# Kernel tuning notes

Measured on AMD Instinct MI355X. Metric: run time of the kernel, lower is better.

## Reference

```python
import jax, jax.numpy as jnp
import numpy as np

N = 500_000    # total nodes across batched ligands
E = 2_000_000  # directed edges (avg degree 4)
G = 16_384     # number of graphs
ND, ED, H, EMB = 44, 12, 64, 128


def setup_inputs() -> dict:
    key = jax.random.key(0)
    ks = jax.random.split(key, 16)

    def w(k, shape, fan_in):
        return jax.random.normal(k, shape, jnp.float32) * (1.0 / np.sqrt(fan_in))

    return {
        "x": jax.random.normal(ks[0], (N, ND), jnp.float32),
        "edge_attr": jax.random.normal(ks[1], (E, ED), jnp.float32),
        "edge_index": jax.random.randint(ks[2], (2, E), 0, N, jnp.int32),
        "batch": jnp.sort(jax.random.randint(ks[3], (N,), 0, G, jnp.int32)),
        # GINEConv 1: edge lin (ED->ND), nn1: ND->64->64
        "el1_w": w(ks[4], (ED, ND), ED), "el1_b": jnp.zeros((ND,), jnp.float32),
        "w1a": w(ks[5], (ND, H), ND),   "b1a": jnp.zeros((H,), jnp.float32),
        "w1b": w(ks[6], (H, H), H),     "b1b": jnp.zeros((H,), jnp.float32),
        # GINEConv 2: edge lin (ED->64), nn2: 64->128->128
        "el2_w": w(ks[7], (ED, H), ED), "el2_b": jnp.zeros((H,), jnp.float32),
        "w2a": w(ks[8], (H, EMB), H),   "b2a": jnp.zeros((EMB,), jnp.float32),
        "w2b": w(ks[9], (EMB, EMB), EMB), "b2b": jnp.zeros((EMB,), jnp.float32),
    }


def _mlp(h, Wa, ba, Wb, bb):
    return jax.nn.relu(h @ Wa + ba) @ Wb + bb


def _gine(x, edge_attr, src, dst, ew, eb, Wa, ba, Wb, bb):
    # message = ReLU(x_j + Linear(edge_attr)); aggregate = scatter-add at target i
    msg = jax.nn.relu(x[src] + edge_attr @ ew + eb)          # [E, d]
    agg = jax.ops.segment_sum(msg, dst, num_segments=x.shape[0])
    # eps = 0 (default, train_eps=False): (1+eps)*x + agg == x + agg
    return _mlp(x + agg, Wa, ba, Wb, bb)


def reference(x, edge_attr, edge_index, batch,
              el1_w, el1_b, w1a, b1a, w1b, b1b,
              el2_w, el2_b, w2a, b2a, w2b, b2b):
    src, dst = edge_index[0], edge_index[1]
    h = jax.nn.relu(_gine(x, edge_attr, src, dst, el1_w, el1_b, w1a, b1a, w1b, b1b))
    h = _gine(h, edge_attr, src, dst, el2_w, el2_b, w2a, b2a, w2b, b2b)
    # global mean pool over graphs
    sums = jax.ops.segment_sum(h, batch, num_segments=G)                 # [G, EMB]
    cnt = jax.ops.segment_sum(jnp.ones((h.shape[0], 1), h.dtype), batch, num_segments=G)
    return sums / jnp.maximum(cnt, 1.0)
```

## Files before the change

### kernel.cpp

```cpp
#include <hip/hip_runtime.h>
#include <hip/hip_bf16.h>

#define NN 500000
#define EE 2000000
#define GG 16384
#define ND 44
#define ED 12
#define HH 64
#define EMB 128
#define NBLK 123
#define NTILE (NN / 16)

typedef __attribute__((ext_vector_type(8))) short bf16x8;
typedef __attribute__((ext_vector_type(4))) float f32x4;
typedef __attribute__((ext_vector_type(2))) _Float16 h2v;

__device__ inline short f2bf(float v) {
    unsigned int x = __builtin_bit_cast(unsigned int, v);
    x += 0x7FFFu + ((x >> 16) & 1u);
    return (short)(x >> 16);
}
__device__ inline unsigned short f2h(float v) {
    return __builtin_bit_cast(unsigned short, (_Float16)v);
}
__device__ inline float h2f(unsigned short s) {
    return (float)__builtin_bit_cast(_Float16, s);
}
__device__ inline unsigned pkh(float a, float b) {
    return (unsigned)f2h(a) | ((unsigned)f2h(b) << 16);
}
__device__ inline float2 upk(unsigned u) {
    return make_float2((float)__builtin_bit_cast(_Float16, (unsigned short)(u & 0xffffu)),
                       (float)__builtin_bit_cast(_Float16, (unsigned short)(u >> 16)));
}
__device__ inline float hdot2(unsigned a, unsigned b, float c) {
#if __has_builtin(__builtin_amdgcn_fdot2)
    return __builtin_amdgcn_fdot2(__builtin_bit_cast(h2v, a),
                                  __builtin_bit_cast(h2v, b), c, false);
#else
    float2 av = upk(a), bv = upk(b);
    return fmaf(av.y, bv.y, fmaf(av.x, bv.x, c));
#endif
}

__device__ inline void wave_lds_fence() {
    asm volatile("s_waitcnt lgkmcnt(0)" ::: "memory");
    __builtin_amdgcn_sched_barrier(0);
}

__global__ __launch_bounds__(256) void prep_weights(
    const float* __restrict__ w1a, const float* __restrict__ w1b,
    const float* __restrict__ w2a, const float* __restrict__ w2b,
    short* __restrict__ o) {
    int t = blockIdx.x * 256 + threadIdx.x;
    if (t < 4096) {
        int n = t >> 6, k = t & 63;
        o[t] = f2bf(k < ND ? w1a[k * HH + n] : 0.f);
    } else if (t < 8192) {
        int u = t - 4096; int n = u >> 6, k = u & 63;
        o[t] = f2bf(w1b[k * HH + n]);
    } else if (t < 16384) {
        int u = t - 8192; int n = u >> 6, k = u & 63;
        o[t] = f2bf(w2a[k * EMB + n]);
    } else if (t < 32768) {
        int u = t - 16384; int n = u >> 7, k = u & 127;
        o[t] = f2bf(w2b[k * EMB + n]);
    }
}

__global__ __launch_bounds__(256) void x_to_h(const float* __restrict__ x,
                                             unsigned short* __restrict__ xh) {
    for (long long t = (long long)(blockIdx.x) * 256 + threadIdx.x;
         t < (long long)NN * 64; t += (long long)gridDim.x * 256) {
        int i = (int)(t >> 6), c = (int)(t & 63);
        xh[t] = (c < ND) ? f2h(x[(size_t)i * ND + c]) : (unsigned short)0;
    }
}

__global__ __launch_bounds__(256) void hist_kernel(const int* __restrict__ ei,
                                                   int* __restrict__ deg) {
    int e = blockIdx.x * 256 + threadIdx.x;
    if (e < EE) atomicAdd(&deg[ei[EE + e]], 1);
}

__global__ __launch_bounds__(256) void scan_reduce(const int* __restrict__ deg,
                                                   int* __restrict__ bsum) {
    int b = blockIdx.x, t = threadIdx.x;
    int base = b * 4096;
    int s = 0;
    for (int i = t; i < 4096; i += 256) {
        int g = base + i;
        if (g < NN) s += deg[g];
    }
#pragma unroll
    for (int off = 32; off; off >>= 1) s += __shfl_xor(s, off);
    __shared__ int ws[4];
    if ((t & 63) == 0) ws[t >> 6] = s;
    __syncthreads();
    if (t == 0) bsum[b] = ws[0] + ws[1] + ws[2] + ws[3];
}

__global__ __launch_bounds__(128) void scan_mid(const int* __restrict__ bsum,
                                                int* __restrict__ boff,
                                                int* __restrict__ rowptr) {
    int t = threadIdx.x;
    int v = (t < NBLK) ? bsum[t] : 0;
    int x = v;
#pragma unroll
    for (int off = 1; off < 64; off <<= 1) {
        int y = __shfl_up(x, off);
        if ((t & 63) >= off) x += y;
    }
    __shared__ int wt[2];
    if ((t & 63) == 63) wt[t >> 6] = x;
    __syncthreads();
    int xx = x + ((t >= 64) ? wt[0] : 0);
    if (t < NBLK) boff[t] = xx - v;
    if (t == 127) rowptr[NN] = xx;
}

__global__ __launch_bounds__(256) void scan_final(const int* __restrict__ deg,
                                                  const int* __restrict__ boff,
                                                  int* __restrict__ rowptr,
                                                  int* __restrict__ cursor) {
    int b = blockIdx.x, t = threadIdx.x;
    int base = b * 4096 + t * 16;
    int loc[16];
    int s = 0;
#pragma unroll
    for (int j = 0; j < 16; ++j) {
        int g = base + j;
        loc[j] = (g < NN) ? deg[g] : 0;
        s += loc[j];
    }
    int xinc = s;
#pragma unroll
    for (int off = 1; off < 64; off <<= 1) {
        int y = __shfl_up(xinc, off);
        if ((t & 63) >= off) xinc += y;
    }
    __shared__ int wt[4];
    if ((t & 63) == 63) wt[t >> 6] = xinc;
    __syncthreads();
    int wv = t >> 6, woff = 0;
#pragma unroll
    for (int k = 0; k < 4; ++k)
        if (k < wv) woff += wt[k];
    int run = boff[b] + woff + (xinc - s);
#pragma unroll
    for (int j = 0; j < 16; ++j) {
        int g = base + j;
        if (g < NN) { rowptr[g] = run; cursor[g] = run; }
        run += loc[j];
    }
}

__global__ __launch_bounds__(256) void scatter_kernel(const int* __restrict__ ei,
                                                      const float* __restrict__ ea,
                                                      int* __restrict__ cursor,
                                                      unsigned int* __restrict__ csr) {
    int e = blockIdx.x * 256 + threadIdx.x;
    if (e < EE) {
        int dst = ei[EE + e];
        const float4* s = (const float4*)(ea + (size_t)e * ED);
        float4 a0 = s[0], a1 = s[1], a2 = s[2];
        uint4 P0, P1;
        P0.x = pkh(a0.x, a0.y); P0.y = pkh(a0.z, a0.w);
        P0.z = pkh(a1.x, a1.y); P0.w = pkh(a1.z, a1.w);
        P1.x = pkh(a2.x, a2.y); P1.y = pkh(a2.z, a2.w);
        P1.z = (unsigned)ei[e];
        P1.w = 0u;
        int pos = atomicAdd(&cursor[dst], 1);
        uint4* d = (uint4*)(csr + (size_t)pos * 8);
        d[0] = P0; d[1] = P1;
    }
}

template <int D>
__global__ __launch_bounds__(256) void agg_gather(
    const unsigned short* __restrict__ xh,
    const unsigned int* __restrict__ cea,
    const float* __restrict__ ew, const float* __restrict__ eb,
    const int* __restrict__ rowptr,
    short* __restrict__ out) {
    int lane = threadIdx.x & 63;
    int wv = threadIdx.x >> 6;
    int i0 = (blockIdx.x * 4 + wv) * 8;
    if (i0 >= NN) return;
    unsigned wp0, wp1, wp2, wp3, wp4, wp5;
    float breg;
    if (D == 64 || lane < D) {
        wp0 = pkh(ew[0 * D + lane], ew[1 * D + lane]);
        wp1 = pkh(ew[2 * D + lane], ew[3 * D + lane]);
        wp2 = pkh(ew[4 * D + lane], ew[5 * D + lane]);
        wp3 = pkh(ew[6 * D + lane], ew[7 * D + lane]);
        wp4 = pkh(ew[8 * D + lane], ew[9 * D + lane]);
        wp5 = pkh(ew[10 * D + lane], ew[11 * D + lane]);
        breg = eb[lane];
    } else {
        wp0 = wp1 = wp2 = wp3 = wp4 = wp5 = 0u; breg = 0.f;
    }
    int rp = (lane <= 8) ? rowptr[i0 + lane] : 0;
    int beg = __builtin_amdgcn_readfirstlane(__builtin_amdgcn_readlane(rp, 0));
    int end = __builtin_amdgcn_readfirstlane(__builtin_amdgcn_readlane(rp, 8));
    int s0 = 0, s1 = 0;
    if (beg + lane < end) s0 = (int)cea[(size_t)(beg + lane) * 8 + 6];
    if (beg + 64 + lane < end) s1 = (int)cea[(size_t)(beg + 64 + lane) * 8 + 6];

    auto SKIPLD = [&](int j) -> float {
        return h2f(xh[(size_t)(i0 + j) * 64 + lane]);
    };

    float acc = 0.f;
    int np = 0;
    int nb = __builtin_amdgcn_readlane(rp, 1);
    float sk = SKIPLD(0);
    while (np < 8 && nb == beg) {
        out[(size_t)(i0 + np) * 64 + lane] = f2bf(sk);
        ++np;
        nb = (np < 8) ? __builtin_amdgcn_readlane(rp, np + 1) : 0x7fffffff;
        sk = (np < 8) ? SKIPLD(np) : 0.f;
    }

    auto LOADE = [&](int pos, uint4& P0, uint2& P1, unsigned short& XR) {
        int p = pos < end ? pos : end - 1;
        int off = p - beg;
        int src;
        if (off < 64)       src = __builtin_amdgcn_readlane(s0, off);
        else if (off < 128) src = __builtin_amdgcn_readlane(s1, off - 64);
        else                src = __builtin_amdgcn_readfirstlane((int)cea[(size_t)p * 8 + 6]);
        P0 = *(const uint4*)(cea + (size_t)p * 8);
        P1 = *(const uint2*)(cea + (size_t)p * 8 + 4);
        XR = xh[(size_t)src * 64 + lane];
    };
    auto CONSUME = [&](int pos, const uint4& P0, const uint2& P1, unsigned short XR) {
        if (pos < end) {
            float elin = breg;
            elin = hdot2(P0.x, wp0, elin);
            elin = hdot2(P0.y, wp1, elin);
            elin = hdot2(P0.z, wp2, elin);
            elin = hdot2(P0.w, wp3, elin);
            elin = hdot2(P1.x, wp4, elin);
            elin = hdot2(P1.y, wp5, elin);
            acc += fmaxf(h2f(XR) + elin, 0.f);
            int p1 = pos + 1;
            if (p1 == nb) {
                do {
                    out[(size_t)(i0 + np) * 64 + lane] = f2bf(acc + sk);
                    acc = 0.f; ++np;
                    nb = (np < 8) ? __builtin_amdgcn_readlane(rp, np + 1) : 0x7fffffff;
                    sk = (np < 8) ? SKIPLD(np) : 0.f;
                } while (p1 == nb);
            }
        }
    };

    if (beg >= end) return;

    uint4 A0, B0, C0, D0, E0, F0, G0, H0;
    uint2 A1, B1, C1, D1, E1, F1, G1, H1;
    unsigned short Ax, Bx, Cx, Dx, Ex, Fx, Gx, Hx;
    int base = beg;
    LOADE(base + 0, A0, A1, Ax);
    LOADE(base + 1, B0, B1, Bx);
    LOADE(base + 2, C0, C1, Cx);
    LOADE(base + 3, D0, D1, Dx);
    LOADE(base + 4, E0, E1, Ex);
    LOADE(base + 5, F0, F1, Fx);
    LOADE(base + 6, G0, G1, Gx);
    LOADE(base + 7, H0, H1, Hx);
    __builtin_amdgcn_sched_barrier(0);
    while (base < end) {
        CONSUME(base + 0, A0, A1, Ax);
        CONSUME(base + 1, B0, B1, Bx);
        LOADE(base + 8, A0, A1, Ax);
        LOADE(base + 9, B0, B1, Bx);
        __builtin_amdgcn_sched_barrier(0);
        if (base + 2 >= end) break;
        CONSUME(base + 2, C0, C1, Cx);
        CONSUME(base + 3, D0, D1, Dx);
        LOADE(base + 10, C0, C1, Cx);
        LOADE(base + 11, D0, D1, Dx);
        __builtin_amdgcn_sched_barrier(0);
        if (base + 4 >= end) break;
        CONSUME(base + 4, E0, E1, Ex);
        CONSUME(base + 5, F0, F1, Fx);
        LOADE(base + 12, E0, E1, Ex);
        LOADE(base + 13, F0, F1, Fx);
        __builtin_amdgcn_sched_barrier(0);
        if (base + 6 >= end) break;
        CONSUME(base + 6, G0, G1, Gx);
        CONSUME(base + 7, H0, H1, Hx);
        LOADE(base + 14, G0, G1, Gx);
        LOADE(base + 15, H0, H1, Hx);
        __builtin_amdgcn_sched_barrier(0);
        base += 8;
    }
}

#define HSTR1 68
__global__ __launch_bounds__(256, 3) void mlp1(
    const short* __restrict__ ain,
    const short* __restrict__ w1a_t, const float* __restrict__ b1a,
    const short* __restrict__ w1b_t, const float* __restrict__ b1b,
    unsigned short* __restrict__ h) {
    __shared__ float hid[4][16 * HSTR1];
    int lane = threadIdx.x & 63;
    int wv = threadIdx.x >> 6;
    int mrow = lane & 15, q = lane >> 4;
    float* hw = hid[wv];

    bf16x8 wa[4][2], wb[4][2];
    float ba[4], bb[4];
#pragma unroll
    for (int nt = 0; nt < 4; ++nt) {
        int n = nt * 16 + mrow;
        ba[nt] = b1a[n]; bb[nt] = b1b[n];
#pragma unroll
        for (int s = 0; s < 2; ++s) {
            wa[nt][s] = *(const bf16x8*)(w1a_t + n * 64 + s * 32 + q * 8);
            wb[nt][s] = *(const bf16x8*)(w1b_t + n * 64 + s * 32 + q * 8);
        }
    }

    int tile = blockIdx.x * 4 + wv;
    int stride = gridDim.x * 4;
    if (tile >= NTILE) return;
    bf16x8 a0 = *(const bf16x8*)(ain + (size_t)(tile * 16 + mrow) * 64 + q * 8);
    bf16x8 a1 = *(const bf16x8*)(ain + (size_t)(tile * 16 + mrow) * 64 + 32 + q * 8);
    while (true) {
        int nxt = tile + stride;
        bool more = nxt < NTILE;
        bf16x8 na0{}, na1{};
        if (more) {
            na0 = *(const bf16x8*)(ain + (size_t)(nxt * 16 + mrow) * 64 + q * 8);
            na1 = *(const bf16x8*)(ain + (size_t)(nxt * 16 + mrow) * 64 + 32 + q * 8);
        }
        int node0 = tile * 16;
#pragma unroll
        for (int nt = 0; nt < 4; ++nt) {
            f32x4 acc = {ba[nt], ba[nt], ba[nt], ba[nt]};
            acc = __builtin_amdgcn_mfma_f32_16x16x32_bf16(a0, wa[nt][0], acc, 0, 0, 0);
            acc = __builtin_amdgcn_mfma_f32_16x16x32_bf16(a1, wa[nt][1], acc, 0, 0, 0);
            int n = nt * 16 + mrow;
#pragma unroll
            for (int r = 0; r < 4; ++r)
                hw[(q * 4 + r) * HSTR1 + n] = fmaxf(acc[r], 0.f);
        }
        wave_lds_fence();
        bf16x8 af2[2];
#pragma unroll
        for (int s = 0; s < 2; ++s) {
            f32x4 v0 = *(const f32x4*)(hw + mrow * HSTR1 + s * 32 + q * 8);
            f32x4 v1 = *(const f32x4*)(hw + mrow * HSTR1 + s * 32 + q * 8 + 4);
#pragma unroll
            for (int j = 0; j < 4; ++j) { af2[s][j] = f2bf(v0[j]); af2[s][j + 4] = f2bf(v1[j]); }
        }
#pragma unroll
        for (int nt = 0; nt < 4; ++nt) {
            f32x4 acc = {bb[nt], bb[nt], bb[nt], bb[nt]};
            acc = __builtin_amdgcn_mfma_f32_16x16x32_bf16(af2[0], wb[nt][0], acc, 0, 0, 0);
            acc = __builtin_amdgcn_mfma_f32_16x16x32_bf16(af2[1], wb[nt][1], acc, 0, 0, 0);
            int n = nt * 16 + mrow;
#pragma unroll
            for (int r = 0; r < 4; ++r)
                h[(size_t)(node0 + q * 4 + r) * HH + n] = f2h(fmaxf(acc[r], 0.f));
        }
        if (!more) break;
        tile = nxt; a0 = na0; a1 = na1;
        wave_lds_fence();
    }
}

#define HSTR2 132
#define WLSTR 136
__global__ __launch_bounds__(256, 2) void mlp2(
    const short* __restrict__ ain,
    const short* __restrict__ w2a_t, const float* __restrict__ b2a,
    const short* __restrict__ w2b_t, const float* __restrict__ b2b,
    const int* __restrict__ batch, float* __restrict__ sums) {
    __shared__ float buf[4][16 * HSTR2];
    __shared__ short wlds[EMB * WLSTR];
    int lane = threadIdx.x & 63;
    int wv = threadIdx.x >> 6;
    int mrow = lane & 15, q = lane >> 4;
    float* bw = buf[wv];

    for (int idx = threadIdx.x * 8; idx < EMB * EMB; idx += 2048) {
        int n = idx >> 7, k = idx & 127;
        *(bf16x8*)(wlds + n * WLSTR + k) = *(const bf16x8*)(w2b_t + idx);
    }

    bf16x8 wa[8][2];
    float ba[8], bb[8];
#pragma unroll
    for (int nt = 0; nt < 8; ++nt) {
        int n = nt * 16 + mrow;
        ba[nt] = b2a[n]; bb[nt] = b2b[n];
#pragma unroll
        for (int s = 0; s < 2; ++s)
            wa[nt][s] = *(const bf16x8*)(w2a_t + n * HH + s * 32 + q * 8);
    }
    __syncthreads();

    int tile = blockIdx.x * 4 + wv;
    int stride = gridDim.x * 4;
    if (tile >= NTILE) return;
    bf16x8 a0 = *(const bf16x8*)(ain + (size_t)(tile * 16 + mrow) * 64 + q * 8);
    bf16x8 a1 = *(const bf16x8*)(ain + (size_t)(tile * 16 + mrow) * 64 + 32 + q * 8);
    int bv = (lane < 16) ? batch[tile * 16 + lane] : 0;
    while (true) {
        int nxt = tile + stride;
        bool more = nxt < NTILE;
        bf16x8 na0{}, na1{};
        int nbv = 0;
        if (more) {
            na0 = *(const bf16x8*)(ain + (size_t)(nxt * 16 + mrow) * 64 + q * 8);
            na1 = *(const bf16x8*)(ain + (size_t)(nxt * 16 + mrow) * 64 + 32 + q * 8);
            nbv = (lane < 16) ? batch[nxt * 16 + lane] : 0;
        }
#pragma unroll
        for (int nt = 0; nt < 8; ++nt) {
            f32x4 acc = {ba[nt], ba[nt], ba[nt], ba[nt]};
            acc = __builtin_amdgcn_mfma_f32_16x16x32_bf16(a0, wa[nt][0], acc, 0, 0, 0);
            acc = __builtin_amdgcn_mfma_f32_16x16x32_bf16(a1, wa[nt][1], acc, 0, 0, 0);
            int n = nt * 16 + mrow;
#pragma unroll
            for (int r = 0; r < 4; ++r)
                bw[(q * 4 + r) * HSTR2 + n] = fmaxf(acc[r], 0.f);
        }
        wave_lds_fence();
        bf16x8 af2[4];
#pragma unroll
        for (int s = 0; s < 4; ++s) {
            f32x4 v0 = *(const f32x4*)(bw + mrow * HSTR2 + s * 32 + q * 8);
            f32x4 v1 = *(const f32x4*)(bw + mrow * HSTR2 + s * 32 + q * 8 + 4);
#pragma unroll
            for (int j = 0; j < 4; ++j) { af2[s][j] = f2bf(v0[j]); af2[s][j + 4] = f2bf(v1[j]); }
        }
#pragma unroll
        for (int nt = 0; nt < 8; ++nt) {
            f32x4 acc = {bb[nt], bb[nt], bb[nt], bb[nt]};
#pragma unroll
            for (int s = 0; s < 4; ++s) {
                bf16x8 bfrag = *(const bf16x8*)(wlds + (nt * 16 + mrow) * WLSTR + s * 32 + q * 8);
                acc = __builtin_amdgcn_mfma_f32_16x16x32_bf16(af2[s], bfrag, acc, 0, 0, 0);
            }
#pragma unroll
            for (int r = 0; r < 4; ++r)
                bw[(q * 4 + r) * HSTR2 + nt * 16 + mrow] = acc[r];
        }
        wave_lds_fence();
#pragma unroll
        for (int cp = 0; cp < 2; ++cp) {
            int col = lane + cp * 64;
            float run = 0.f;
            int bprev = __shfl(bv, 0);
            for (int i = 0; i < 16; ++i) {
                int bg = __shfl(bv, i);
                if (bg != bprev) {
                    atomicAdd(&sums[bprev * EMB + col], run);
                    run = 0.f; bprev = bg;
                }
                run += bw[i * HSTR2 + col];
            }
            atomicAdd(&sums[bprev * EMB + col], run);
        }
        if (!more) break;
        tile = nxt; a0 = na0; a1 = na1; bv = nbv;
        wave_lds_fence();
    }
}

__global__ __launch_bounds__(128) void finalize(
    const float* __restrict__ sums, const int* __restrict__ batch,
    float* __restrict__ out) {
    int g = blockIdx.x;
    __shared__ int cnt_s;
    if (threadIdx.x == 0) {
        int lo = 0, hi = NN;
        while (lo < hi) { int mid = (lo + hi) >> 1; if (batch[mid] < g) lo = mid + 1; else hi = mid; }
        int lo2 = lo, hi2 = NN;
        while (lo2 < hi2) { int mid = (lo2 + hi2) >> 1; if (batch[mid] < g + 1) lo2 = mid + 1; else hi2 = mid; }
        cnt_s = lo2 - lo;
    }
    __syncthreads();
    int c = cnt_s > 1 ? cnt_s : 1;
    out[g * EMB + threadIdx.x] = sums[g * EMB + threadIdx.x] / (float)c;
}

extern "C" void kernel_launch(void* const* d_in, const int* in_sizes, int n_in,
                              void* d_out, int out_size, void* d_ws, size_t ws_size,
                              hipStream_t stream) {
    const float* x    = (const float*)d_in[0];
    const float* ea   = (const float*)d_in[1];
    const int*   ei   = (const int*)d_in[2];
    const int*   batch= (const int*)d_in[3];
    const float* el1w = (const float*)d_in[4];
    const float* el1b = (const float*)d_in[5];
    const float* w1a  = (const float*)d_in[6];
    const float* b1a  = (const float*)d_in[7];
    const float* w1b  = (const float*)d_in[8];
    const float* b1b  = (const float*)d_in[9];
    const float* el2w = (const float*)d_in[10];
    const float* el2b = (const float*)d_in[11];
    const float* w2a  = (const float*)d_in[12];
    const float* b2a  = (const float*)d_in[13];
    const float* w2b  = (const float*)d_in[14];
    const float* b2b  = (const float*)d_in[15];

    char* ws = (char*)d_ws;
    short*          aggout = (short*)ws;
    unsigned short* hbuf16 = (unsigned short*)(ws + 64000000);
    unsigned int*   csr32  = (unsigned int*)(ws + 128000000);
    int*   rowptr = (int*)(ws + 192000000);
    int*   cursor = (int*)(ws + 194000064);
    int*   deg    = (int*)(ws + 196000064);
    int*   bsum   = (int*)(ws + 198000064);
    int*   boff   = (int*)(ws + 198000576);
    float* sums   = (float*)(ws + 198001088);
    short* wts    = (short*)(ws + 206389696);
    unsigned short* xh = (unsigned short*)(ws + 208000000);
    short* w1a_t = wts;
    short* w1b_t = wts + 4096;
    short* w2a_t = wts + 8192;
    short* w2b_t = wts + 16384;

    hipMemsetAsync(deg, 0, (size_t)NN * 4, stream);
    hipMemsetAsync(sums, 0, (size_t)GG * EMB * 4, stream);

    prep_weights<<<128, 256, 0, stream>>>(w1a, w1b, w2a, w2b, wts);
    x_to_h<<<4096, 256, 0, stream>>>(x, xh);
    hist_kernel<<<(EE + 255) / 256, 256, 0, stream>>>(ei, deg);
    scan_reduce<<<NBLK, 256, 0, stream>>>(deg, bsum);
    scan_mid<<<1, 128, 0, stream>>>(bsum, boff, rowptr);
    scan_final<<<NBLK, 256, 0, stream>>>(deg, boff, rowptr, cursor);
    scatter_kernel<<<(EE + 255) / 256, 256, 0, stream>>>(ei, ea, cursor, csr32);
    agg_gather<ND><<<NN / 32, 256, 0, stream>>>(xh, csr32, el1w, el1b, rowptr, aggout);
    mlp1<<<1024, 256, 0, stream>>>(aggout, w1a_t, b1a, w1b_t, b1b, hbuf16);
    agg_gather<HH><<<NN / 32, 256, 0, stream>>>(hbuf16, csr32, el2w, el2b, rowptr, aggout);
    mlp2<<<512, 256, 0, stream>>>(aggout, w2a_t, b2a, w2b_t, b2b, batch, sums);
    finalize<<<GG, 128, 0, stream>>>(sums, batch, (float*)d_out);
}
```

Baseline: 791.3 us.

## Stage edge records in lanes per 64-edge chunk and vectorize x conversion

The gather kernel now loads each 64-edge chunk's CSR records once, spread across the wave's lanes with coalesced 16-byte loads, and broadcasts edge attributes via readlane. Before, every lane reloaded the full 24-byte record for every edge. Separately, x_to_h uses 8-wide vector loads and stores, one thread per 8 output columns, with a matching grid size. The cost is six extra readlanes per edge and a pipeline restart at each chunk boundary.

Result: faster. 773.9 us (-2.2%).

```diff
diff --git a/kernel.cpp b/kernel.cpp
--- a/kernel.cpp
+++ b/kernel.cpp
@@ -13,6 +13,7 @@
 
 typedef __attribute__((ext_vector_type(8))) short bf16x8;
 typedef __attribute__((ext_vector_type(4))) float f32x4;
+typedef __attribute__((ext_vector_type(8))) unsigned short u16x8;
 typedef __attribute__((ext_vector_type(2))) _Float16 h2v;
 
 __device__ inline short f2bf(float v) {
@@ -70,11 +71,24 @@
 
 __global__ __launch_bounds__(256) void x_to_h(const float* __restrict__ x,
                                              unsigned short* __restrict__ xh) {
-    for (long long t = (long long)(blockIdx.x) * 256 + threadIdx.x;
-         t < (long long)NN * 64; t += (long long)gridDim.x * 256) {
-        int i = (int)(t >> 6), c = (int)(t & 63);
-        xh[t] = (c < ND) ? f2h(x[(size_t)i * ND + c]) : (unsigned short)0;
-    }
+    int t = blockIdx.x * 256 + threadIdx.x;
+    int i = t >> 3, g = t & 7;
+    int c0 = g * 8;
+    u16x8 o = {0, 0, 0, 0, 0, 0, 0, 0};
+    if (c0 < ND) {
+        const float* rx = x + (size_t)i * ND + c0;
+        if (c0 + 8 <= ND) {
+            f32x4 v0 = *(const f32x4*)rx;
+            f32x4 v1 = *(const f32x4*)(rx + 4);
+#pragma unroll
+            for (int j = 0; j < 4; ++j) { o[j] = f2h(v0[j]); o[j + 4] = f2h(v1[j]); }
+        } else {
+            f32x4 v0 = *(const f32x4*)rx;
+#pragma unroll
+            for (int j = 0; j < 4; ++j) o[j] = f2h(v0[j]);
+        }
+    }
+    *(u16x8*)(xh + (size_t)i * 64 + c0) = o;
 }
 
 __global__ __launch_bounds__(256) void hist_kernel(const int* __restrict__ ei,
@@ -203,9 +217,6 @@
     int rp = (lane <= 8) ? rowptr[i0 + lane] : 0;
     int beg = __builtin_amdgcn_readfirstlane(__builtin_amdgcn_readlane(rp, 0));
     int end = __builtin_amdgcn_readfirstlane(__builtin_amdgcn_readlane(rp, 8));
-    int s0 = 0, s1 = 0;
-    if (beg + lane < end) s0 = (int)cea[(size_t)(beg + lane) * 8 + 6];
-    if (beg + 64 + lane < end) s1 = (int)cea[(size_t)(beg + 64 + lane) * 8 + 6];
 
     auto SKIPLD = [&](int j) -> float {
         return h2f(xh[(size_t)(i0 + j) * 64 + lane]);
@@ -222,79 +233,93 @@
         sk = (np < 8) ? SKIPLD(np) : 0.f;
     }
 
-    auto LOADE = [&](int pos, uint4& P0, uint2& P1, unsigned short& XR) {
-        int p = pos < end ? pos : end - 1;
-        int off = p - beg;
-        int src;
-        if (off < 64)       src = __builtin_amdgcn_readlane(s0, off);
-        else if (off < 128) src = __builtin_amdgcn_readlane(s1, off - 64);
-        else                src = __builtin_amdgcn_readfirstlane((int)cea[(size_t)p * 8 + 6]);
-        P0 = *(const uint4*)(cea + (size_t)p * 8);
-        P1 = *(const uint2*)(cea + (size_t)p * 8 + 4);
-        XR = xh[(size_t)src * 64 + lane];
-    };
-    auto CONSUME = [&](int pos, const uint4& P0, const uint2& P1, unsigned short XR) {
-        if (pos < end) {
-            float elin = breg;
-            elin = hdot2(P0.x, wp0, elin);
-            elin = hdot2(P0.y, wp1, elin);
-            elin = hdot2(P0.z, wp2, elin);
-            elin = hdot2(P0.w, wp3, elin);
-            elin = hdot2(P1.x, wp4, elin);
-            elin = hdot2(P1.y, wp5, elin);
-            acc += fmaxf(h2f(XR) + elin, 0.f);
-            int p1 = pos + 1;
-            if (p1 == nb) {
-                do {
-                    out[(size_t)(i0 + np) * 64 + lane] = f2bf(acc + sk);
-                    acc = 0.f; ++np;
-                    nb = (np < 8) ? __builtin_amdgcn_readlane(rp, np + 1) : 0x7fffffff;
-                    sk = (np < 8) ? SKIPLD(np) : 0.f;
-                } while (p1 == nb);
+    if (beg >= end) return;
+
+    int c0 = beg;
+    while (c0 < end) {
+        int cend = (end < c0 + 64) ? end : c0 + 64;
+        unsigned qa0 = 0, qa1 = 0, qa2 = 0, qa3 = 0, qa4 = 0, qa5 = 0;
+        int qsrc = 0;
+        if (c0 + lane < end) {
+            const uint4* rp4 = (const uint4*)(cea + (size_t)(c0 + lane) * 8);
+            uint4 a = rp4[0], b = rp4[1];
+            qa0 = a.x; qa1 = a.y; qa2 = a.z; qa3 = a.w; qa4 = b.x; qa5 = b.y;
+            qsrc = (int)b.z;
+        }
+
+        auto LOADE = [&](int pos, unsigned short& XR) {
+            int p = pos < cend ? pos : cend - 1;
+            int off = p - c0;
+            int src = __builtin_amdgcn_readlane(qsrc, off);
+            XR = xh[(size_t)src * 64 + lane];
+        };
+        auto CONSUME = [&](int pos, unsigned short XR) {
+            if (pos < cend) {
+                int off = pos - c0;
+                unsigned a0 = __builtin_amdgcn_readlane(qa0, off);
+                unsigned a1 = __builtin_amdgcn_readlane(qa1, off);
+                unsigned a2 = __builtin_amdgcn_readlane(qa2, off);
+                unsigned a3 = __builtin_amdgcn_readlane(qa3, off);
+                unsigned a4 = __builtin_amdgcn_readlane(qa4, off);
+                unsigned a5 = __builtin_amdgcn_readlane(qa5, off);
+                float elin = breg;
+                elin = hdot2(a0, wp0, elin);
+                elin = hdot2(a1, wp1, elin);
+                elin = hdot2(a2, wp2, elin);
+                elin = hdot2(a3, wp3, elin);
+                elin = hdot2(a4, wp4, elin);
+                elin = hdot2(a5, wp5, elin);
+                acc += fmaxf(h2f(XR) + elin, 0.f);
+                int p1 = pos + 1;
+                if (p1 == nb) {
+                    do {
+                        out[(size_t)(i0 + np) * 64 + lane] = f2bf(acc + sk);
+                        acc = 0.f; ++np;
+                        nb = (np < 8) ? __builtin_amdgcn_readlane(rp, np + 1) : 0x7fffffff;
+                        sk = (np < 8) ? SKIPLD(np) : 0.f;
+                    } while (p1 == nb);
+                }
             }
-        }
-    };
-
-    if (beg >= end) return;
-
-    uint4 A0, B0, C0, D0, E0, F0, G0, H0;
-    uint2 A1, B1, C1, D1, E1, F1, G1, H1;
-    unsigned short Ax, Bx, Cx, Dx, Ex, Fx, Gx, Hx;
-    int base = beg;
-    LOADE(base + 0, A0, A1, Ax);
-    LOADE(base + 1, B0, B1, Bx);
-    LOADE(base + 2, C0, C1, Cx);
-    LOADE(base + 3, D0, D1, Dx);
-    LOADE(base + 4, E0, E1, Ex);
-    LOADE(base + 5, F0, F1, Fx);
-    LOADE(base + 6, G0, G1, Gx);
-    LOADE(base + 7, H0, H1, Hx);
-    __builtin_amdgcn_sched_barrier(0);
-    while (base < end) {
-        CONSUME(base + 0, A0, A1, Ax);
-        CONSUME(base + 1, B0, B1, Bx);
-        LOADE(base + 8, A0, A1, Ax);
-        LOADE(base + 9, B0, B1, Bx);
+        };
+
+        unsigned short XA, XB, XC, XD, XE, XF, XG, XH;
+        LOADE(c0 + 0, XA);
+        LOADE(c0 + 1, XB);
+        LOADE(c0 + 2, XC);
+        LOADE(c0 + 3, XD);
+        LOADE(c0 + 4, XE);
+        LOADE(c0 + 5, XF);
+        LOADE(c0 + 6, XG);
+        LOADE(c0 + 7, XH);
         __builtin_amdgcn_sched_barrier(0);
-        if (base + 2 >= end) break;
-        CONSUME(base + 2, C0, C1, Cx);
-        CONSUME(base + 3, D0, D1, Dx);
-        LOADE(base + 10, C0, C1, Cx);
-        LOADE(base + 11, D0, D1, Dx);
-        __builtin_amdgcn_sched_barrier(0);
-        if (base + 4 >= end) break;
-        CONSUME(base + 4, E0, E1, Ex);
-        CONSUME(base + 5, F0, F1, Fx);
-        LOADE(base + 12, E0, E1, Ex);
-        LOADE(base + 13, F0, F1, Fx);
-        __builtin_amdgcn_sched_barrier(0);
-        if (base + 6 >= end) break;
-        CONSUME(base + 6, G0, G1, Gx);
-        CONSUME(base + 7, H0, H1, Hx);
-        LOADE(base + 14, G0, G1, Gx);
-        LOADE(base + 15, H0, H1, Hx);
-        __builtin_amdgcn_sched_barrier(0);
-        base += 8;
+        int base = c0;
+        while (base < cend) {
+            CONSUME(base + 0, XA);
+            CONSUME(base + 1, XB);
+            LOADE(base + 8, XA);
+            LOADE(base + 9, XB);
+            __builtin_amdgcn_sched_barrier(0);
+            if (base + 2 >= cend) break;
+            CONSUME(base + 2, XC);
+            CONSUME(base + 3, XD);
+            LOADE(base + 10, XC);
+            LOADE(base + 11, XD);
+            __builtin_amdgcn_sched_barrier(0);
+            if (base + 4 >= cend) break;
+            CONSUME(base + 4, XE);
+            CONSUME(base + 5, XF);
+            LOADE(base + 12, XE);
+            LOADE(base + 13, XF);
+            __builtin_amdgcn_sched_barrier(0);
+            if (base + 6 >= cend) break;
+            CONSUME(base + 6, XG);
+            CONSUME(base + 7, XH);
+            LOADE(base + 14, XG);
+            LOADE(base + 15, XH);
+            __builtin_amdgcn_sched_barrier(0);
+            base += 8;
+        }
+        c0 = cend;
     }
 }
 
@@ -530,7 +555,7 @@
     hipMemsetAsync(sums, 0, (size_t)GG * EMB * 4, stream);
 
     prep_weights<<<128, 256, 0, stream>>>(w1a, w1b, w2a, w2b, wts);
-    x_to_h<<<4096, 256, 0, stream>>>(x, xh);
+    x_to_h<<<15625, 256, 0, stream>>>(x, xh);
     hist_kernel<<<(EE + 255) / 256, 256, 0, stream>>>(ei, deg);
     scan_reduce<<<NBLK, 256, 0, stream>>>(deg, bsum);
     scan_mid<<<1, 128, 0, stream>>>(bsum, boff, rowptr);
```
